# Performance work log

Measured on AMD Instinct MI355X. Metric: run time of the kernel, lower is better.

The kernel has to match this reference:

```python
import jax, jax.numpy as jnp
import numpy as np

WIN = 8
SHIFT = 4
HEADS = 8


def _rel_pos_index(ws):
    # static numpy computation matching the torch buffer
    coords = np.stack(np.meshgrid(np.arange(ws), np.arange(ws), indexing='ij'))  # (2, ws, ws)
    cf = coords.reshape(2, -1)                      # (2, N)
    rel = cf[:, :, None] - cf[:, None, :]           # (2, N, N)
    rel = rel.transpose(1, 2, 0).copy()             # (N, N, 2)
    rel[:, :, 0] += ws - 1
    rel[:, :, 1] += ws - 1
    rel[:, :, 0] *= 2 * ws - 1
    return rel.sum(-1)                              # (N, N) int


def _attn_mask(H, W, ws, ss):
    # static shift mask, numpy (shapes are static under jit)
    img = np.zeros((H, W))
    cnt = 0
    sl = (slice(0, -ws), slice(-ws, -ss), slice(-ss, None))
    for h in sl:
        for w in sl:
            img[h, w] = cnt
            cnt += 1
    mw = img.reshape(H // ws, ws, W // ws, ws).transpose(0, 2, 1, 3).reshape(-1, ws * ws)
    diff = mw[:, None, :] - mw[:, :, None]          # (nW, N, N), matches unsqueeze(1)-unsqueeze(2)
    return np.where(diff != 0, -100.0, 0.0).astype(np.float32)


def setup_inputs() -> dict:
    key = jax.random.key(0)
    ks = jax.random.split(key, 6)
    B, C, H, W = 4, 192, 256, 256
    return {
        'x': jax.random.normal(ks[0], (B, C, H, W), jnp.float32),
        'qkv_w': jax.random.normal(ks[1], (3 * C, C), jnp.float32) * 0.02,
        'qkv_b': jnp.zeros((3 * C,), jnp.float32),
        'proj_w': jax.random.normal(ks[2], (C, C), jnp.float32) * 0.02,
        'proj_b': jnp.zeros((C,), jnp.float32),
        'rpb_table': jax.random.normal(ks[3], ((2 * WIN - 1) ** 2, HEADS), jnp.float32) * 0.02,
    }


def reference(x, qkv_w, qkv_b, proj_w, proj_b, rpb_table):
    B, C, H, W = x.shape
    ws, ss, h = WIN, SHIFT, HEADS
    N = ws * ws
    hd = C // h
    scale = hd ** -0.5

    xh = jnp.transpose(x, (0, 2, 3, 1))                       # (B,H,W,C)
    xs = jnp.roll(xh, shift=(-ss, -ss), axis=(1, 2))          # cyclic shift
    # window partition -> (B*nW, N, C)
    xw = xs.reshape(B, H // ws, ws, W // ws, ws, C).transpose(0, 1, 3, 2, 4, 5).reshape(-1, N, C)

    qkv = xw @ qkv_w.T + qkv_b                                # (B_, N, 3C)
    qkv = qkv.reshape(-1, N, 3, h, hd).transpose(2, 0, 3, 1, 4)
    q, k, v = qkv[0], qkv[1], qkv[2]                          # (B_, h, N, hd)

    attn = (q * scale) @ jnp.swapaxes(k, -2, -1)              # (B_, h, N, N)

    rpi = _rel_pos_index(ws)
    bias = rpb_table[rpi.reshape(-1)].reshape(N, N, h).transpose(2, 0, 1)  # (h, N, N)
    attn = attn + bias[None]

    mask = jnp.asarray(_attn_mask(H, W, ws, ss))              # (nW, N, N)
    nW = mask.shape[0]
    attn = attn.reshape(B, nW, h, N, N) + mask[None, :, None]
    attn = jax.nn.softmax(attn.reshape(-1, h, N, N), axis=-1)

    out = (attn @ v).transpose(0, 2, 1, 3).reshape(-1, N, C)  # (B_, N, C)
    out = out @ proj_w.T + proj_b

    # window reverse
    out = out.reshape(B, H // ws, W // ws, ws, ws, C).transpose(0, 1, 3, 2, 4, 5).reshape(B, H, W, C)
    out = jnp.roll(out, shift=(ss, ss), axis=(1, 2))          # reverse shift
    return x + jnp.transpose(out, (0, 3, 1, 2))               # residual, (B,C,H,W)
```

## Files before the change

kernel.cpp:

```cpp
#include <hip/hip_runtime.h>


typedef short short8 __attribute__((ext_vector_type(8)));
typedef float f32x4 __attribute__((ext_vector_type(4)));
typedef unsigned short us4 __attribute__((ext_vector_type(4)));

#define XB_OFF   0
#define KQ_OFF   12288
#define VT_OFF   24576
#define PB_OFF   24576
#define RPB_OFF  38400
#define QB_OFF   40200
#define LDS_BYTES 81552

#define WBF_BYTES 294912u
#define Y_FLOATS_PER_WIN 12288
#define Y_BYTES (4096ull * 49152ull)
#define WS_NEED (WBF_BYTES + Y_BYTES)

__device__ __forceinline__ unsigned short f2bfu(float f) {
  union { float f; unsigned u; } v; v.f = f;
  unsigned u = v.u;
  u += 0x7fffu + ((u >> 16) & 1u);
  return (unsigned short)(u >> 16);
}
__device__ __forceinline__ float bfu2f(unsigned short s) {
  union { unsigned u; float f; } v; v.u = ((unsigned)s) << 16;
  return v.f;
}

__device__ __forceinline__ int swzX(int t, int c) {
  return (((t >> 4) * 6 + (c >> 5)) << 9) | (((c >> 3) & 3) << 7) |
         ((t & 15) << 3) | (c & 7);
}
__device__ __forceinline__ int swzH(int i, int h, int g, int n, int j) {
  return (((i * 8 + h) * 3 + g) << 7) | (n << 3) | j;
}

__global__ void prep_weights(const float* __restrict__ qkv_w,
                             const float* __restrict__ proj_w,
                             unsigned short* __restrict__ wbf) {
  int d = blockIdx.x * 512 + threadIdx.x;
  int j    = d & 7;
  int lane = (d >> 3) & 63;
  int kk   = (d >> 9) % 6;
  int tile = d / 3072;
  int n16 = lane & 15, q4 = lane >> 4;
  int col = kk * 32 + q4 * 8 + j;
  float v = (tile < 36) ? qkv_w[(tile * 16 + n16) * 192 + col]
                        : proj_w[((tile - 36) * 16 + n16) * 192 + col];
  wbf[d] = f2bfu(v);
}

template <bool TOY>
__global__ __launch_bounds__(512, 4) void winattn_kernel(
    const float* __restrict__ x, const float* __restrict__ qkv_b,
    const float* __restrict__ proj_b, const float* __restrict__ rpb,
    const unsigned short* __restrict__ wbf, float* __restrict__ dst)
{
  extern __shared__ __align__(16) char smem[];
  unsigned short* lds = (unsigned short*)smem;

  const int tid  = threadIdx.x;
  const int lane = tid & 63;
  const int wave = tid >> 6;
  const int n16  = lane & 15;
  const int q4   = lane >> 4;

  const int blk = blockIdx.x;
  const int L   = (blk & 7) * 512 + (blk >> 3);
  const int b    = L >> 10;
  const int wIdx = L & 1023;
  const int wr   = wIdx >> 5;
  const int wc   = wIdx & 31;

  {
    const int trow = wave;
    const int c3 = lane >> 3, w3 = lane & 7;
    const int hh  = (wr * 8 + 4 + trow) & 255;
    const int ww  = (wc * 8 + 4 + w3) & 255;
    const int t   = trow * 8 + w3;
    #pragma unroll
    for (int it = 0; it < 12; it++) {
      const int c = it * 16 + c3 * 2;
      const float* xp = x + (((size_t)(b * 192 + c)) << 16) + (hh << 8) + ww;
      float v0 = xp[0];
      float v1 = xp[65536];
      unsigned pk = (unsigned)f2bfu(v0) | ((unsigned)f2bfu(v1) << 16);
      *(unsigned*)(lds + XB_OFF + swzX(t, c)) = pk;
    }
    for (int i = tid; i < 1800; i += 512)
      lds[RPB_OFF + (i & 7) * 225 + (i >> 3)] = f2bfu(rpb[i]);
    for (int i = tid; i < 576; i += 512)
      lds[QB_OFF + i] = f2bfu(qkv_b[i]);
  }
  __syncthreads();

  {
    short8 bx[4][6];
    #pragma unroll
    for (int tt = 0; tt < 4; tt++)
      #pragma unroll
      for (int kk = 0; kk < 6; kk++)
        bx[tt][kk] = *(const short8*)(lds + XB_OFF + ((tt * 6 + kk) * 64 + lane) * 8);

    #pragma unroll 1
    for (int ot = wave; ot < 24; ot += 8) {
      f32x4 acc[4] = {{0,0,0,0},{0,0,0,0},{0,0,0,0},{0,0,0,0}};
      #pragma unroll
      for (int kk = 0; kk < 6; kk++) {
        short8 af = *(const short8*)(wbf + ((ot + 12) * 6 + kk) * 512 + lane * 8);
        #pragma unroll
        for (int tt = 0; tt < 4; tt++)
          acc[tt] = __builtin_amdgcn_mfma_f32_16x16x32_bf16(af, bx[tt][kk], acc[tt], 0, 0, 0);
      }
      const int ob = (ot + 12) * 16 + q4 * 4;
      const float b0 = bfu2f(lds[QB_OFF + ob + 0]);
      const float b1 = bfu2f(lds[QB_OFF + ob + 1]);
      const float b2 = bfu2f(lds[QB_OFF + ob + 2]);
      const float b3 = bfu2f(lds[QB_OFF + ob + 3]);
      if (ot < 12) {
        const int kc = ot * 16 + q4 * 4;
        const int hk = kc / 24, g = (kc >> 3) % 3, j0 = kc & 7;
        #pragma unroll
        for (int tt = 0; tt < 4; tt++) {
          us4 hv = { f2bfu(acc[tt][0] + b0), f2bfu(acc[tt][1] + b1),
                     f2bfu(acc[tt][2] + b2), f2bfu(acc[tt][3] + b3) };
          *(us4*)(lds + KQ_OFF + swzH(tt, hk, g, n16, j0)) = hv;
        }
      } else {
        const int vc = (ot - 12) * 16 + q4 * 4;
        #pragma unroll
        for (int tt = 0; tt < 4; tt++) {
          const int t = tt * 16 + n16;
          lds[VT_OFF + (vc + 0) * 72 + t] = f2bfu(acc[tt][0] + b0);
          lds[VT_OFF + (vc + 1) * 72 + t] = f2bfu(acc[tt][1] + b1);
          lds[VT_OFF + (vc + 2) * 72 + t] = f2bfu(acc[tt][2] + b2);
          lds[VT_OFF + (vc + 3) * 72 + t] = f2bfu(acc[tt][3] + b3);
        }
      }
    }
  }
  __syncthreads();

  const int h = wave;
  const short8 zero8 = {0,0,0,0,0,0,0,0};
  short8 kb[4], vb[2][2];
  {
    #pragma unroll
    for (int i = 0; i < 4; i++)
      kb[i] = (q4 < 3) ? *(const short8*)(lds + KQ_OFF + swzH(i, h, q4, n16, 0))
                       : zero8;
    #pragma unroll
    for (int nc = 0; nc < 2; nc++)
      #pragma unroll
      for (int kk = 0; kk < 2; kk++)
        vb[nc][kk] = (nc * 16 + n16 < 24)
          ? *(const short8*)(lds + VT_OFF + (h * 24 + nc * 16 + n16) * 72 + kk * 32 + q4 * 8)
          : zero8;
  }
  __syncthreads();

  {
    #pragma unroll 1
    for (int ot = wave; ot < 12; ot += 8) {
      f32x4 acc[4] = {{0,0,0,0},{0,0,0,0},{0,0,0,0},{0,0,0,0}};
      #pragma unroll
      for (int kk = 0; kk < 6; kk++) {
        short8 af = *(const short8*)(wbf + (ot * 6 + kk) * 512 + lane * 8);
        #pragma unroll
        for (int tt = 0; tt < 4; tt++) {
          short8 bxk = *(const short8*)(lds + XB_OFF + ((tt * 6 + kk) * 64 + lane) * 8);
          acc[tt] = __builtin_amdgcn_mfma_f32_16x16x32_bf16(af, bxk, acc[tt], 0, 0, 0);
        }
      }
      const int ob = ot * 16 + q4 * 4;
      const float b0 = bfu2f(lds[QB_OFF + ob + 0]);
      const float b1 = bfu2f(lds[QB_OFF + ob + 1]);
      const float b2 = bfu2f(lds[QB_OFF + ob + 2]);
      const float b3 = bfu2f(lds[QB_OFF + ob + 3]);
      const int qc = ot * 16 + q4 * 4;
      const int hq = qc / 24, g = (qc >> 3) % 3, j0 = qc & 7;
      #pragma unroll
      for (int tt = 0; tt < 4; tt++) {
        us4 hv = { f2bfu(acc[tt][0] + b0), f2bfu(acc[tt][1] + b1),
                   f2bfu(acc[tt][2] + b2), f2bfu(acc[tt][3] + b3) };
        *(us4*)(lds + KQ_OFF + swzH(tt, hq, g, n16, j0)) = hv;
      }
    }
  }
  __syncthreads();

  {
    short8 qa[4];
    #pragma unroll
    for (int i = 0; i < 4; i++)
      qa[i] = (q4 < 3) ? *(const short8*)(lds + KQ_OFF + swzH(i, h, q4, n16, 0))
                       : zero8;
    __syncthreads();

    const float scale = 0.20412414523193154f;
    unsigned short* Pw = lds + PB_OFF + wave * 1152;
    const unsigned short* rh = lds + RPB_OFF + h * 225;
    int cr[4], cc[4], clab[4];
    #pragma unroll
    for (int nj = 0; nj < 4; nj++) {
      int col = nj * 16 + n16;
      cr[nj] = col >> 3; cc[nj] = col & 7;
      int hs = wr * 8 + cr[nj], wsc = wc * 8 + cc[nj];
      int lh = (hs < 248) ? 0 : (hs < 252 ? 1 : 2);
      int lw = (wsc < 248) ? 0 : (wsc < 252 ? 1 : 2);
      clab[nj] = lh * 3 + lw;
    }
    #pragma unroll
    for (int mi = 0; mi < 4; mi++) {
      f32x4 smi[4];
      #pragma unroll
      for (int nj = 0; nj < 4; nj++) {
        f32x4 z = {0,0,0,0};
        smi[nj] = __builtin_amdgcn_mfma_f32_16x16x32_bf16(qa[mi], kb[nj], z, 0, 0, 0);
      }
      #pragma unroll
      for (int r = 0; r < 4; r++) {
        int row = mi * 16 + q4 * 4 + r;
        int r1 = row >> 3, c1 = row & 7;
        int hs = wr * 8 + r1, wsc = wc * 8 + c1;
        int lh = (hs < 248) ? 0 : (hs < 252 ? 1 : 2);
        int lw = (wsc < 248) ? 0 : (wsc < 252 ? 1 : 2);
        int rlab = lh * 3 + lw;
        float vals[4];
        float mx = -1e30f;
        #pragma unroll
        for (int nj = 0; nj < 4; nj++) {
          float v = smi[nj][r] * scale
                  + bfu2f(rh[(r1 - cr[nj] + 7) * 15 + (c1 - cc[nj] + 7)])
                  + ((rlab == clab[nj]) ? 0.0f : -100.0f);
          vals[nj] = v;
          mx = fmaxf(mx, v);
        }
        mx = fmaxf(mx, __shfl_xor(mx, 1));
        mx = fmaxf(mx, __shfl_xor(mx, 2));
        mx = fmaxf(mx, __shfl_xor(mx, 4));
        mx = fmaxf(mx, __shfl_xor(mx, 8));
        float sum = 0.f;
        #pragma unroll
        for (int nj = 0; nj < 4; nj++) { float p = __expf(vals[nj] - mx); vals[nj] = p; sum += p; }
        sum += __shfl_xor(sum, 1);
        sum += __shfl_xor(sum, 2);
        sum += __shfl_xor(sum, 4);
        sum += __shfl_xor(sum, 8);
        float inv = 1.0f / sum;
        #pragma unroll
        for (int nj = 0; nj < 4; nj++)
          Pw[(q4 * 4 + r) * 72 + nj * 16 + n16] = f2bfu(vals[nj] * inv);
      }
      short8 pa0 = *(const short8*)(Pw + n16 * 72 + q4 * 8);
      short8 pa1 = *(const short8*)(Pw + n16 * 72 + 32 + q4 * 8);
      #pragma unroll
      for (int nc = 0; nc < 2; nc++) {
        f32x4 a = {0,0,0,0};
        a = __builtin_amdgcn_mfma_f32_16x16x32_bf16(pa0, vb[nc][0], a, 0, 0, 0);
        a = __builtin_amdgcn_mfma_f32_16x16x32_bf16(pa1, vb[nc][1], a, 0, 0, 0);
        const int ch = nc * 16 + n16;
        if (ch < 24) {
          const int c = h * 24 + ch;
          #pragma unroll
          for (int r = 0; r < 4; r++) {
            const int t = mi * 16 + q4 * 4 + r;
            lds[KQ_OFF + swzX(t, c)] = f2bfu(a[r]);
          }
        }
      }
    }
  }
  __syncthreads();

  {
    short8 bo[4][6];
    #pragma unroll
    for (int tt = 0; tt < 4; tt++)
      #pragma unroll
      for (int kk = 0; kk < 6; kk++)
        bo[tt][kk] = *(const short8*)(lds + KQ_OFF + ((tt * 6 + kk) * 64 + lane) * 8);

    #pragma unroll 1
    for (int ot = wave; ot < 12; ot += 8) {
      f32x4 acc[4] = {{0,0,0,0},{0,0,0,0},{0,0,0,0},{0,0,0,0}};
      #pragma unroll
      for (int kk = 0; kk < 6; kk++) {
        short8 af = *(const short8*)(wbf + ((36 + ot) * 6 + kk) * 512 + lane * 8);
        #pragma unroll
        for (int tt = 0; tt < 4; tt++)
          acc[tt] = __builtin_amdgcn_mfma_f32_16x16x32_bf16(af, bo[tt][kk], acc[tt], 0, 0, 0);
      }
      if constexpr (TOY) {
        float* yw = dst + (size_t)L * Y_FLOATS_PER_WIN;
        #pragma unroll
        for (int r = 0; r < 4; r++) {
          const int o = ot * 16 + q4 * 4 + r;
          const float pb = proj_b[o];
          #pragma unroll
          for (int tt = 0; tt < 4; tt++) {
            const int t = tt * 16 + n16;
            yw[o * 64 + t] = bfu2f(lds[XB_OFF + swzX(t, o)]) + acc[tt][r] + pb;
          }
        }
      } else {
        #pragma unroll
        for (int r = 0; r < 4; r++) {
          const int o = ot * 16 + q4 * 4 + r;
          const float pb = proj_b[o];
          const size_t cbase = ((size_t)(b * 192 + o)) << 16;
          #pragma unroll
          for (int tt = 0; tt < 4; tt++) {
            const int t = tt * 16 + n16;
            const int hh = (wr * 8 + (t >> 3) + 4) & 255;
            const int ww = (wc * 8 + (t & 7) + 4) & 255;
            dst[cbase + (hh << 8) + ww] = bfu2f(lds[XB_OFF + swzX(t, o)]) + acc[tt][r] + pb;
          }
        }
      }
    }
  }
}

__global__ __launch_bounds__(512) void unshift_kernel(
    const float* __restrict__ Y, float* __restrict__ out)
{
  const int bid = blockIdx.x;
  const int cg = bid & 7;
  const int wr = (bid >> 3) & 31;
  const int b  = bid >> 8;
  const size_t winrow = ((size_t)(b * 32 + wr)) * 32;

  for (int i = threadIdx.x; i < 24 * 2048; i += 512) {
    const int c_rel = i >> 11;
    const int rem   = i & 2047;
    const int trow  = rem >> 8;
    const int wp    = rem & 255;
    const int c     = cg * 24 + c_rel;
    const float v = Y[(winrow + (wp >> 3)) * Y_FLOATS_PER_WIN + c * 64 + trow * 8 + (wp & 7)];
    const int hh = (wr * 8 + trow + 4) & 255;
    const int ww = (wp + 4) & 255;
    out[(((size_t)(b * 192 + c)) << 16) + (hh << 8) + ww] = v;
  }
}

extern "C" void kernel_launch(void* const* d_in, const int* in_sizes, int n_in,
                              void* d_out, int out_size, void* d_ws, size_t ws_size,
                              hipStream_t stream) {
  const float* x      = (const float*)d_in[0];
  const float* qkv_w  = (const float*)d_in[1];
  const float* qkv_b  = (const float*)d_in[2];
  const float* proj_w = (const float*)d_in[3];
  const float* proj_b = (const float*)d_in[4];
  const float* rpb    = (const float*)d_in[5];
  float* out = (float*)d_out;
  unsigned short* wbf = (unsigned short*)d_ws;

  hipFuncSetAttribute(reinterpret_cast<const void*>(&winattn_kernel<true>),
                      hipFuncAttributeMaxDynamicSharedMemorySize, LDS_BYTES);
  hipFuncSetAttribute(reinterpret_cast<const void*>(&winattn_kernel<false>),
                      hipFuncAttributeMaxDynamicSharedMemorySize, LDS_BYTES);

  prep_weights<<<dim3(288), dim3(512), 0, stream>>>(qkv_w, proj_w, wbf);

  if (ws_size >= (size_t)WS_NEED) {
    float* Y = (float*)((char*)d_ws + WBF_BYTES);
    winattn_kernel<true><<<dim3(4096), dim3(512), LDS_BYTES, stream>>>(
        x, qkv_b, proj_b, rpb, wbf, Y);
    unshift_kernel<<<dim3(1024), dim3(512), 0, stream>>>(Y, out);
  } else {
    winattn_kernel<false><<<dim3(4096), dim3(512), LDS_BYTES, stream>>>(
        x, qkv_b, proj_b, rpb, wbf, out);
  }
}
```

Baseline: 651.1 us.

## Stream B fragments from LDS in MFMA loops and vectorize unshift copy

The QKV and projection GEMM loops no longer preload all 24 B fragments into registers. Each fragment is now read from LDS right before its MFMA, which lowers register pressure, and the occupancy hint is changed to amdgpu_waves_per_eu(4,4). The unshift kernel now moves 8 contiguous floats per thread with two 16-byte loads and stores instead of scalar accesses. The trade-off is more LDS reads inside the inner loop, since each fragment is re-read once per output tile iteration, in exchange for higher occupancy and wider global memory transactions.

```diff
diff --git a/kernel.cpp b/kernel.cpp
--- a/kernel.cpp
+++ b/kernel.cpp
@@ -53,7 +53,9 @@
 }
 
 template <bool TOY>
-__global__ __launch_bounds__(512, 4) void winattn_kernel(
+__global__ __launch_bounds__(512)
+__attribute__((amdgpu_waves_per_eu(4, 4)))
+void winattn_kernel(
     const float* __restrict__ x, const float* __restrict__ qkv_b,
     const float* __restrict__ proj_b, const float* __restrict__ rpb,
     const unsigned short* __restrict__ wbf, float* __restrict__ dst)
@@ -97,13 +99,6 @@
   __syncthreads();
 
   {
-    short8 bx[4][6];
-    #pragma unroll
-    for (int tt = 0; tt < 4; tt++)
-      #pragma unroll
-      for (int kk = 0; kk < 6; kk++)
-        bx[tt][kk] = *(const short8*)(lds + XB_OFF + ((tt * 6 + kk) * 64 + lane) * 8);
-
     #pragma unroll 1
     for (int ot = wave; ot < 24; ot += 8) {
       f32x4 acc[4] = {{0,0,0,0},{0,0,0,0},{0,0,0,0},{0,0,0,0}};
@@ -111,8 +106,10 @@
       for (int kk = 0; kk < 6; kk++) {
         short8 af = *(const short8*)(wbf + ((ot + 12) * 6 + kk) * 512 + lane * 8);
         #pragma unroll
-        for (int tt = 0; tt < 4; tt++)
-          acc[tt] = __builtin_amdgcn_mfma_f32_16x16x32_bf16(af, bx[tt][kk], acc[tt], 0, 0, 0);
+        for (int tt = 0; tt < 4; tt++) {
+          short8 bxk = *(const short8*)(lds + XB_OFF + ((tt * 6 + kk) * 64 + lane) * 8);
+          acc[tt] = __builtin_amdgcn_mfma_f32_16x16x32_bf16(af, bxk, acc[tt], 0, 0, 0);
+        }
       }
       const int ob = (ot + 12) * 16 + q4 * 4;
       const float b0 = bfu2f(lds[QB_OFF + ob + 0]);
@@ -276,13 +273,6 @@
   __syncthreads();
 
   {
-    short8 bo[4][6];
-    #pragma unroll
-    for (int tt = 0; tt < 4; tt++)
-      #pragma unroll
-      for (int kk = 0; kk < 6; kk++)
-        bo[tt][kk] = *(const short8*)(lds + KQ_OFF + ((tt * 6 + kk) * 64 + lane) * 8);
-
     #pragma unroll 1
     for (int ot = wave; ot < 12; ot += 8) {
       f32x4 acc[4] = {{0,0,0,0},{0,0,0,0},{0,0,0,0},{0,0,0,0}};
@@ -290,8 +280,10 @@
       for (int kk = 0; kk < 6; kk++) {
         short8 af = *(const short8*)(wbf + ((36 + ot) * 6 + kk) * 512 + lane * 8);
         #pragma unroll
-        for (int tt = 0; tt < 4; tt++)
-          acc[tt] = __builtin_amdgcn_mfma_f32_16x16x32_bf16(af, bo[tt][kk], acc[tt], 0, 0, 0);
+        for (int tt = 0; tt < 4; tt++) {
+          short8 bok = *(const short8*)(lds + KQ_OFF + ((tt * 6 + kk) * 64 + lane) * 8);
+          acc[tt] = __builtin_amdgcn_mfma_f32_16x16x32_bf16(af, bok, acc[tt], 0, 0, 0);
+        }
       }
       if constexpr (TOY) {
         float* yw = dst + (size_t)L * Y_FLOATS_PER_WIN;
@@ -333,16 +325,21 @@
   const int b  = bid >> 8;
   const size_t winrow = ((size_t)(b * 32 + wr)) * 32;
 
-  for (int i = threadIdx.x; i < 24 * 2048; i += 512) {
-    const int c_rel = i >> 11;
-    const int rem   = i & 2047;
-    const int trow  = rem >> 8;
-    const int wp    = rem & 255;
+  #pragma unroll
+  for (int it = 0; it < 12; it++) {
+    const int i = it * 512 + threadIdx.x;
+    const int c_rel = i >> 8;
+    const int rem   = i & 255;
+    const int trow  = rem >> 5;
+    const int k     = rem & 31;
     const int c     = cg * 24 + c_rel;
-    const float v = Y[(winrow + (wp >> 3)) * Y_FLOATS_PER_WIN + c * 64 + trow * 8 + (wp & 7)];
+    const float* src = Y + (winrow + k) * Y_FLOATS_PER_WIN + c * 64 + trow * 8;
+    f32x4 v0 = *(const f32x4*)(src);
+    f32x4 v1 = *(const f32x4*)(src + 4);
     const int hh = (wr * 8 + trow + 4) & 255;
-    const int ww = (wp + 4) & 255;
-    out[(((size_t)(b * 192 + c)) << 16) + (hh << 8) + ww] = v;
+    float* drow = out + (((size_t)(b * 192 + c)) << 16) + (hh << 8);
+    *(f32x4*)(drow + ((k * 8 + 4) & 255)) = v0;
+    *(f32x4*)(drow + ((k * 8 + 8) & 255)) = v1;
   }
 }
 
```

Result: faster. 597.0 us (-8.3%).
